# Performance work log

Measured on AMD Instinct MI355X. Metric: run time of the kernel, lower is better.

The kernel has to match this reference:

```python
import jax, jax.numpy as jnp
import numpy as np

B, MQ, MK = 8, 512, 2048
Q_DIM, KV_DIM = 1024, 256
H = 8
QKC, VC = 1024, 1024
DQ, DV = QKC // H, VC // H
EPS = 1e-5  # nn.LayerNorm default


def _layer_norm(x, w, b):
    m = jnp.mean(x, axis=-1, keepdims=True)
    v = jnp.var(x, axis=-1, keepdims=True)
    return (x - m) * jax.lax.rsqrt(v + EPS) * w + b


def setup_inputs() -> dict:
    key = jax.random.key(0)
    ks = jax.random.split(key, 12)
    hidden_states = jax.random.normal(ks[0], (B, MQ, Q_DIM), dtype=jnp.float32)
    inputs = jax.random.normal(ks[1], (B, MK, KV_DIM), dtype=jnp.float32)
    # ragged per-batch kv lengths -> prefix-valid mask (matches keys[i, :n] packing)
    lengths = jax.random.randint(ks[2], (B,), MK // 4, MK + 1)
    inputs_mask = (jnp.arange(MK)[None, :] < lengths[:, None]).astype(jnp.int32)
    s = 0.02
    return {
        "hidden_states": hidden_states,
        "inputs": inputs,
        "inputs_mask": inputs_mask,
        "ln1_w": jnp.ones((Q_DIM,), jnp.float32),
        "ln1_b": jnp.zeros((Q_DIM,), jnp.float32),
        "ln2_w": jnp.ones((KV_DIM,), jnp.float32),
        "ln2_b": jnp.zeros((KV_DIM,), jnp.float32),
        "Wq": s * jax.random.normal(ks[3], (Q_DIM, QKC), dtype=jnp.float32),
        "bq": jnp.zeros((QKC,), jnp.float32),
        "Wk": s * jax.random.normal(ks[4], (KV_DIM, QKC), dtype=jnp.float32),
        "bk": jnp.zeros((QKC,), jnp.float32),
        "Wv": s * jax.random.normal(ks[5], (KV_DIM, VC), dtype=jnp.float32),
        "bv": jnp.zeros((VC,), jnp.float32),
    }


def reference(hidden_states, inputs, inputs_mask, ln1_w, ln1_b, ln2_w, ln2_b,
              Wq, bq, Wk, bk, Wv, bv):
    hs = _layer_norm(hidden_states, ln1_w, ln1_b)      # [B, MQ, Q_DIM]
    kv = _layer_norm(inputs, ln2_w, ln2_b)             # [B, MK, KV_DIM]

    q = (hs @ Wq + bq).reshape(B, MQ, H, DQ)           # [B, MQ, H, DQ]
    k = (kv @ Wk + bk).reshape(B, MK, H, DQ)           # [B, MK, H, DQ]
    v = (kv @ Wv + bv).reshape(B, MK, H, DV)           # [B, MK, H, DV]

    scores = jnp.einsum("bqhd,bkhd->bhqk", q, k) / jnp.sqrt(jnp.float32(DQ))
    mask_f = inputs_mask.astype(scores.dtype)          # [B, MK]
    neg = jnp.finfo(scores.dtype).min
    scores = scores + (1.0 - mask_f)[:, None, None, :] * neg
    probs = jax.nn.softmax(scores, axis=-1)            # [B, H, MQ, MK]

    ctx = jnp.einsum("bhqk,bkhd->bqhd", probs, v)      # [B, MQ, H, DV]
    return ctx.reshape(B, MQ, H * DV)
```

## Files before the change

kernel.cpp:

```cpp
#include <hip/hip_runtime.h>

#define DI __device__ __forceinline__

typedef _Float16 f16x8 __attribute__((ext_vector_type(8)));
typedef _Float16 f16x4 __attribute__((ext_vector_type(4)));
typedef float    f32x4 __attribute__((ext_vector_type(4)));

namespace {

constexpr int kB  = 8;
constexpr int kMQ = 512;
constexpr int kMK = 2048;
constexpr int kQKC = 1024;
constexpr int kVC  = 1024;

DI void gload16(const void* g, void* l) {
  __builtin_amdgcn_global_load_lds(
      (const __attribute__((address_space(1))) void*)g,
      (__attribute__((address_space(3))) void*)l, 16, 0, 0);
}

DI f32x4 mfma16(f16x8 a, f16x8 b, f32x4 c) {
  return __builtin_amdgcn_mfma_f32_16x16x32_f16(a, b, c, 0, 0, 0);
}

DI f32x4 mfma16k16(f16x4 a, f16x4 b, f32x4 c) {
  return __builtin_amdgcn_mfma_f32_16x16x16f16(a, b, c, 0, 0, 0);
}

template<int K, int N>
DI void transpose_dev(const float* __restrict__ W, _Float16* __restrict__ WT,
                      int bid, float (*t)[65]) {
  int nt = bid % (N / 64), kt = bid / (N / 64);
  int k0 = kt * 64, n0 = nt * 64;
  int tid = threadIdx.x;
#pragma unroll
  for (int j = 0; j < 16; ++j) {
    int e = tid + j * 256;
    int r = e >> 6, c = e & 63;
    t[r][c] = W[(size_t)(k0 + r) * N + n0 + c];
  }
  __syncthreads();
#pragma unroll
  for (int j = 0; j < 16; ++j) {
    int e = tid + j * 256;
    int r = e >> 6, c = e & 63;
    WT[(size_t)(n0 + r) * K + k0 + c] = (_Float16)t[c][r];
  }
}

DI void ln1024_dev(const float* __restrict__ x, const float* __restrict__ w,
                   const float* __restrict__ bb, _Float16* __restrict__ y,
                   int row, float* red) {
  int tid = threadIdx.x;
  const float4* xr = (const float4*)(x + (size_t)row * 1024);
  float4 v = xr[tid];
  float s = v.x + v.y + v.z + v.w;
  float q = v.x * v.x + v.y * v.y + v.z * v.z + v.w * v.w;
#pragma unroll
  for (int m = 32; m; m >>= 1) { s += __shfl_xor(s, m); q += __shfl_xor(q, m); }
  if ((tid & 63) == 0) { red[tid >> 6] = s; red[4 + (tid >> 6)] = q; }
  __syncthreads();
  s = red[0] + red[1] + red[2] + red[3];
  q = red[4] + red[5] + red[6] + red[7];
  float mean = s * (1.0f / 1024.0f);
  float var = q * (1.0f / 1024.0f) - mean * mean;
  float inv = rsqrtf(var + 1e-5f);
  f16x4 o;
  const float* wp = w + tid * 4;
  const float* bp = bb + tid * 4;
  o[0] = (_Float16)((v.x - mean) * inv * wp[0] + bp[0]);
  o[1] = (_Float16)((v.y - mean) * inv * wp[1] + bp[1]);
  o[2] = (_Float16)((v.z - mean) * inv * wp[2] + bp[2]);
  o[3] = (_Float16)((v.w - mean) * inv * wp[3] + bp[3]);
  *(f16x4*)(y + (size_t)row * 1024 + tid * 4) = o;
}

DI void ln256_dev(const float* __restrict__ x, const float* __restrict__ w,
                  const float* __restrict__ bb, _Float16* __restrict__ y, int bid) {
  int tid = threadIdx.x;
  int lane = tid & 63, wv = tid >> 6;
  size_t row = (size_t)bid * 4 + wv;
  const float4* xr = (const float4*)(x + row * 256);
  float4 v = xr[lane];
  float s = v.x + v.y + v.z + v.w;
  float q = v.x * v.x + v.y * v.y + v.z * v.z + v.w * v.w;
#pragma unroll
  for (int m = 32; m; m >>= 1) { s += __shfl_xor(s, m); q += __shfl_xor(q, m); }
  float mean = s * (1.0f / 256.0f);
  float var = q * (1.0f / 256.0f) - mean * mean;
  float inv = rsqrtf(var + 1e-5f);
  f16x4 o;
  const float* wp = w + lane * 4;
  const float* bp = bb + lane * 4;
  o[0] = (_Float16)((v.x - mean) * inv * wp[0] + bp[0]);
  o[1] = (_Float16)((v.y - mean) * inv * wp[1] + bp[1]);
  o[2] = (_Float16)((v.z - mean) * inv * wp[2] + bp[2]);
  o[3] = (_Float16)((v.w - mean) * inv * wp[3] + bp[3]);
  *(f16x4*)(y + row * 256 + lane * 4) = o;
}

__global__ __launch_bounds__(256) void prep_all(
    const float* __restrict__ Wq, const float* __restrict__ Wk, const float* __restrict__ Wv,
    _Float16* __restrict__ WqT, _Float16* __restrict__ WkT, _Float16* __restrict__ WvT,
    const float* __restrict__ hs, const float* __restrict__ ln1w, const float* __restrict__ ln1b,
    _Float16* __restrict__ hsln,
    const float* __restrict__ xin, const float* __restrict__ ln2w, const float* __restrict__ ln2b,
    _Float16* __restrict__ kvln,
    const int* __restrict__ msk, int* __restrict__ work) {
  __shared__ float tbuf[64][65];
  int bid = blockIdx.x;
  if (bid < 256) {
    transpose_dev<1024, 1024>(Wq, WqT, bid, tbuf);
  } else if (bid < 320) {
    transpose_dev<256, 1024>(Wk, WkT, bid - 256, tbuf);
  } else if (bid < 384) {
    transpose_dev<256, 1024>(Wv, WvT, bid - 320, tbuf);
  } else if (bid < 4480) {
    ln1024_dev(hs, ln1w, ln1b, hsln, bid - 384, (float*)tbuf);
  } else if (bid < 8576) {
    ln256_dev(xin, ln2w, ln2b, kvln, bid - 4480);
  } else {
    int* wbuf = (int*)tbuf;
    int t = threadIdx.x;
    int b = t >> 5, tile = t & 31;
    wbuf[t] = (msk[b * kMK + tile * 64] != 0) ? 1 : 0;
    __syncthreads();
    if (t < 8) {
      int s = 0;
      for (int i = 0; i < 32; ++i) s += wbuf[t * 32 + i];
      wbuf[256 + t] = s;
    }
    __syncthreads();
    if (t == 0) {
      int ord[8];
      for (int i = 0; i < 8; ++i) ord[i] = i;
      for (int i = 1; i < 8; ++i) {
        int o = ord[i], j = i;
        while (j > 0 && wbuf[256 + ord[j - 1]] < wbuf[256 + o]) { ord[j] = ord[j - 1]; --j; }
        ord[j] = o;
      }
      for (int i = 0; i < 8; ++i) wbuf[264 + i] = ord[i];
    }
    __syncthreads();
#pragma unroll
    for (int k = 0; k < 4; ++k) {
      int p = t + k * 256;
      int s = p >> 7, h = p & 7, qh = (p >> 3) & 15;
      int qt = qh >> 1, half = qh & 1;
      int bb = wbuf[264 + s];
      work[p] = (bb * 8 + h) | (qt << 6) | (half << 9);
    }
  }
}

template<int M, int N, int K, bool BIAS_ROW, int MMODE>
DI void gemm_dev(const _Float16* __restrict__ A, const _Float16* __restrict__ Bt,
                 const float* __restrict__ bias, const int* __restrict__ msk,
                 _Float16* __restrict__ C, int bid,
                 _Float16 (*As)[128 * 64], _Float16 (*Bs)[128 * 64]) {
  int tid = threadIdx.x, lane = tid & 63;
  int w = tid >> 6, wr = w >> 1, wc = w & 1;
  constexpr int NT = N / 128;
  constexpr int KT = K / 64;
  int mt = bid / NT, nt = bid % NT;
  if constexpr (MMODE == 1) { if (msk[mt * 128] == 0) return; }
  if constexpr (MMODE == 2) { if (msk[nt * 128] == 0) return; }
  const int l15 = lane & 15, l4 = lane >> 4;

  f32x4 acc[4][4] = {};

  const int rS = tid >> 3;
  const int cpS = tid & 7;

  auto stage = [&](int kt, int bufi) {
#pragma unroll
    for (int j = 0; j < 4; ++j) {
      int rr = rS + j * 32;
      int cg = cpS ^ (rr & 7);
      gload16(A  + ((size_t)(mt * 128 + rr) * K + kt * 64 + cg * 8),
              (char*)As[bufi] + j * 4096 + tid * 16);
      gload16(Bt + ((size_t)(nt * 128 + rr) * K + kt * 64 + cg * 8),
              (char*)Bs[bufi] + j * 4096 + tid * 16);
    }
  };

  stage(0, 0);
  __syncthreads();

  for (int kt = 0; kt < KT; ++kt) {
    int cur = kt & 1;
    if (kt + 1 < KT) stage(kt + 1, cur ^ 1);
#pragma unroll
    for (int ss = 0; ss < 2; ++ss) {
      f16x8 a[4], b[4];
#pragma unroll
      for (int m = 0; m < 4; ++m) {
        int ra = wr * 64 + m * 16 + l15;
        int cl = ss * 4 + l4;
        a[m] = *(const f16x8*)((const char*)As[cur] + ra * 128 + ((cl ^ (ra & 7)) << 4));
        int rb = wc * 64 + m * 16 + l15;
        b[m] = *(const f16x8*)((const char*)Bs[cur] + rb * 128 + ((cl ^ (rb & 7)) << 4));
      }
#pragma unroll
      for (int m = 0; m < 4; ++m)
#pragma unroll
        for (int n = 0; n < 4; ++n)
          acc[m][n] = mfma16(a[m], b[n], acc[m][n]);
    }
    __syncthreads();
  }

#pragma unroll
  for (int m = 0; m < 4; ++m) {
#pragma unroll
    for (int n = 0; n < 4; ++n) {
      int gi0 = mt * 128 + wr * 64 + m * 16 + l4 * 4;
      int gj  = nt * 128 + wc * 64 + n * 16 + l15;
#pragma unroll
      for (int r = 0; r < 4; ++r) {
        int gi = gi0 + r;
        float v = acc[m][n][r] + (BIAS_ROW ? bias[gi] : bias[gj]);
        C[(size_t)gi * N + gj] = (_Float16)v;
      }
    }
  }
}

__global__ __launch_bounds__(256) void gemm_all(
    const _Float16* __restrict__ hsln, const _Float16* __restrict__ WqT,
    const float* __restrict__ bq, _Float16* __restrict__ qbf,
    const _Float16* __restrict__ kvln, const _Float16* __restrict__ WkT,
    const float* __restrict__ bk, _Float16* __restrict__ kbf,
    const _Float16* __restrict__ WvT, const float* __restrict__ bv,
    _Float16* __restrict__ vT, const int* __restrict__ msk) {
  __shared__ _Float16 As[2][128 * 64];
  __shared__ _Float16 Bs[2][128 * 64];
  int bid = blockIdx.x;
  if (bid < 256) {
    gemm_dev<4096, 1024, 1024, false, 0>(hsln, WqT, bq, nullptr, qbf, bid, As, Bs);
  } else if (bid < 1280) {
    gemm_dev<16384, 1024, 256, false, 1>(kvln, WkT, bk, msk, kbf, bid - 256, As, Bs);
  } else {
    gemm_dev<1024, 16384, 256, true, 2>(WvT, kvln, bv, msk, vT, bid - 1280, As, Bs);
  }
}

__global__ __launch_bounds__(256, 2) void attn_kernel(const _Float16* __restrict__ qm,
                                                      const _Float16* __restrict__ km,
                                                      const _Float16* __restrict__ vT,
                                                      const int* __restrict__ msk,
                                                      const int* __restrict__ work,
                                                      _Float16* __restrict__ pO,
                                                      float* __restrict__ pML) {
  __shared__ _Float16 Ks[2][64 * 128];
  __shared__ _Float16 Vst[2][128 * 64];

  int tid = threadIdx.x, lane = tid & 63, w = tid >> 6;
  int v = work[blockIdx.x];
  int bh = v & 63, qt = (v >> 6) & 7, half = (v >> 9) & 1;
  int h = bh & 7, b = bh >> 3;
  const int l15 = lane & 15, l4 = lane >> 4;

  int vld = (lane < 32) ? msk[b * kMK + lane * 64] : 0;
  int ntiles = __popcll(__ballot(vld != 0));
  int lv = msk[b * kMK + (ntiles - 1) * 64 + lane];
  int lastlen = __popcll(__ballot(lv != 0));

  int h1 = (ntiles + 1) >> 1;
  int t0 = half ? h1 : 0;
  int t1 = half ? ntiles : h1;

  f16x8 qf[4];
#pragma unroll
  for (int kc = 0; kc < 4; ++kc)
    qf[kc] = *(const f16x8*)(qm +
        (size_t)(b * kMQ + qt * 64 + w * 16 + l15) * kQKC +
        h * 128 + kc * 32 + l4 * 8);

  f32x4 o[8] = {};
  float rm = -1e30f, rl = 0.0f;

  const float sl2 = 0.08838834764831845f * 1.4426950408889634f;

  const int rK = tid >> 4, cpK = tid & 15;
  const int rV = tid >> 3, cpV = tid & 7;

  auto stage = [&](int kt, int bufi) {
#pragma unroll
    for (int j = 0; j < 4; ++j) {
      int rr = rK + j * 16;
      int cg = cpK ^ (rr & 7);
      gload16(km + (size_t)(b * kMK + kt * 64 + rr) * kQKC + h * 128 + cg * 8,
              (char*)Ks[bufi] + j * 4096 + tid * 16);
    }
#pragma unroll
    for (int j = 0; j < 4; ++j) {
      int dv = rV + j * 32;
      int cg = cpV ^ (dv & 7);
      gload16(vT + (size_t)(h * 128 + dv) * (kB * kMK) + (size_t)b * kMK + kt * 64 + cg * 8,
              (char*)Vst[bufi] + j * 4096 + tid * 16);
    }
  };

  stage(t0, 0);
  __syncthreads();

  for (int kt = t0; kt < t1; ++kt) {
    int cur = (kt - t0) & 1;
    if (kt + 1 < t1) stage(kt + 1, cur ^ 1);

    f32x4 sc[4] = {};
    __builtin_amdgcn_s_setprio(1);
#pragma unroll
    for (int kc = 0; kc < 4; ++kc) {
      f16x8 kb[4];
#pragma unroll
      for (int kf = 0; kf < 4; ++kf) {
        int rr = kf * 16 + l15;
        int cl = kc * 4 + l4;
        kb[kf] = *(const f16x8*)((const char*)Ks[cur] + rr * 256 + ((cl ^ (rr & 7)) << 4));
      }
#pragma unroll
      for (int kf = 0; kf < 4; ++kf)
        sc[kf] = mfma16(kb[kf], qf[kc], sc[kf]);
    }
    __builtin_amdgcn_s_setprio(0);

    if (kt == ntiles - 1) {
#pragma unroll
      for (int kf = 0; kf < 4; ++kf)
#pragma unroll
        for (int r = 0; r < 4; ++r)
          if (kf * 16 + l4 * 4 + r >= lastlen) sc[kf][r] = -3e38f;
    }

    float mx = sc[0][0];
#pragma unroll
    for (int kf = 0; kf < 4; ++kf)
#pragma unroll
      for (int r = 0; r < 4; ++r) mx = fmaxf(mx, sc[kf][r]);
    mx = fmaxf(mx, __shfl_xor(mx, 16));
    mx = fmaxf(mx, __shfl_xor(mx, 32));
    float al = 1.0f;
    if (__any(mx > rm)) {
      float nm = fmaxf(rm, mx);
      al = __builtin_amdgcn_exp2f((rm - nm) * sl2);
      rm = nm;
#pragma unroll
      for (int n = 0; n < 8; ++n)
#pragma unroll
        for (int r = 0; r < 4; ++r) o[n][r] *= al;
    }
    float nms = rm * sl2;
    float ts = 0.0f;
#pragma unroll
    for (int kf = 0; kf < 4; ++kf)
#pragma unroll
      for (int r = 0; r < 4; ++r) {
        float p = __builtin_amdgcn_exp2f(sc[kf][r] * sl2 - nms);
        sc[kf][r] = p;
        ts += p;
      }
    ts += __shfl_xor(ts, 16);
    ts += __shfl_xor(ts, 32);
    rl = rl * al + ts;

    f16x4 pb[4];
#pragma unroll
    for (int kf = 0; kf < 4; ++kf)
#pragma unroll
      for (int r = 0; r < 4; ++r) pb[kf][r] = (_Float16)sc[kf][r];

    __builtin_amdgcn_s_setprio(1);
#pragma unroll
    for (int n = 0; n < 8; ++n) {
      int dv = n * 16 + l15;
#pragma unroll
      for (int kf = 0; kf < 4; ++kf) {
        int phys = (kf * 2 + (l4 >> 1)) ^ (l15 & 7);
        f16x4 vb = *(const f16x4*)((const char*)Vst[cur] +
                                   dv * 128 + (phys << 4) + (l4 & 1) * 8);
        o[n] = mfma16k16(vb, pb[kf], o[n]);
      }
    }
    __builtin_amdgcn_s_setprio(0);
    __syncthreads();
  }

  int item = bh * 16 + qt * 2 + half;
  _Float16* po = pO + (size_t)item * 8192;
  int qr = w * 16 + l15;
#pragma unroll
  for (int n = 0; n < 8; ++n) {
    f16x4 st;
#pragma unroll
    for (int r = 0; r < 4; ++r) st[r] = (_Float16)o[n][r];
    *(f16x4*)(po + qr * 128 + n * 16 + l4 * 4) = st;
  }
  if (l4 == 0) {
    pML[(item * 64 + qr) * 2 + 0] = rm;
    pML[(item * 64 + qr) * 2 + 1] = rl;
  }
}

__global__ __launch_bounds__(256) void combine_kernel(const _Float16* __restrict__ pO,
                                                      const float* __restrict__ pML,
                                                      float* __restrict__ out) {
  int cid = blockIdx.x;
  int bh = cid & 63, qt = cid >> 6;
  int h = bh & 7, b = bh >> 3;
  int t = threadIdx.x;
  int q = t >> 2, c = t & 3;
  const float sl2 = 0.08838834764831845f * 1.4426950408889634f;

  int i1 = bh * 16 + qt * 2, i2 = i1 + 1;
  float m1 = pML[(i1 * 64 + q) * 2 + 0], l1 = pML[(i1 * 64 + q) * 2 + 1];
  float m2 = pML[(i2 * 64 + q) * 2 + 0], l2 = pML[(i2 * 64 + q) * 2 + 1];
  float m = fmaxf(m1, m2);
  float w1 = __builtin_amdgcn_exp2f((m1 - m) * sl2);
  float w2 = __builtin_amdgcn_exp2f((m2 - m) * sl2);
  float inv = 1.0f / (l1 * w1 + l2 * w2);
  w1 *= inv; w2 *= inv;

  const _Float16* p1 = pO + (size_t)i1 * 8192 + q * 128;
  const _Float16* p2 = pO + (size_t)i2 * 8192 + q * 128;
  float* orow = out + ((size_t)b * kMQ + qt * 64 + q) * kVC + h * 128;
#pragma unroll
  for (int j = 0; j < 4; ++j) {
    int col = c * 32 + j * 8;
    f16x8 a = *(const f16x8*)(p1 + col);
    f16x8 bb = *(const f16x8*)(p2 + col);
    f32x4 o0, o1;
#pragma unroll
    for (int r = 0; r < 4; ++r) {
      o0[r] = (float)a[r] * w1 + (float)bb[r] * w2;
      o1[r] = (float)a[4 + r] * w1 + (float)bb[4 + r] * w2;
    }
    *(f32x4*)(orow + col) = o0;
    *(f32x4*)(orow + col + 4) = o1;
  }
}

}

extern "C" void kernel_launch(void* const* d_in, const int* in_sizes, int n_in,
                              void* d_out, int out_size, void* d_ws, size_t ws_size,
                              hipStream_t stream) {
  (void)in_sizes; (void)n_in; (void)out_size; (void)ws_size;
  const float* hs   = (const float*)d_in[0];
  const float* xin  = (const float*)d_in[1];
  const int*   msk  = (const int*)d_in[2];
  const float* ln1w = (const float*)d_in[3];
  const float* ln1b = (const float*)d_in[4];
  const float* ln2w = (const float*)d_in[5];
  const float* ln2b = (const float*)d_in[6];
  const float* Wq   = (const float*)d_in[7];
  const float* bq   = (const float*)d_in[8];
  const float* Wk   = (const float*)d_in[9];
  const float* bk   = (const float*)d_in[10];
  const float* Wv   = (const float*)d_in[11];
  const float* bv   = (const float*)d_in[12];
  float* out = (float*)d_out;

  char* ws = (char*)d_ws;
  _Float16* qbf  = (_Float16*)(ws + 0);
  _Float16* kbf  = (_Float16*)(ws + 8388608);
  _Float16* vT   = (_Float16*)(ws + 41943040);
  _Float16* hsln = (_Float16*)(ws + 75497472);
  _Float16* kvln = (_Float16*)(ws + 83886080);
  _Float16* WqT  = (_Float16*)(ws + 92274688);
  _Float16* WkT  = (_Float16*)(ws + 94371840);
  _Float16* WvT  = (_Float16*)(ws + 94896128);
  int*      work = (int*)(ws + 95420416);
  _Float16* pO   = hsln;
  float*    pML  = (float*)WqT;

  prep_all<<<8577, 256, 0, stream>>>(Wq, Wk, Wv, WqT, WkT, WvT,
                                     hs, ln1w, ln1b, hsln,
                                     xin, ln2w, ln2b, kvln,
                                     msk, work);
  gemm_all<<<2304, 256, 0, stream>>>(hsln, WqT, bq, qbf,
                                     kvln, WkT, bk, kbf,
                                     WvT, bv, vT, msk);
  attn_kernel<<<1024, 256, 0, stream>>>(qbf, kbf, vT, msk, work, pO, pML);
  combine_kernel<<<512, 256, 0, stream>>>(pO, pML, out);
}
```

Measured before the change: 123.0 us.

## Fuse split-K combine into attention via atomic counter; read V directly from global

The separate combine kernel is removed. Whichever of the two split halves finishes last, detected through an atomic counter that prep_all zeroes, merges both partial outputs inside the attention kernel. V tiles are no longer staged through LDS; each lane reads its f16x4 V fragments straight from global memory (vT). This halves LDS use, which allows launch bounds of 4 blocks per SM. It saves one kernel launch and the LDS copy, at the cost of uncoalesced, strided global V reads that depend on cache hits, plus fence and atomic overhead.

```diff
diff --git a/kernel.cpp b/kernel.cpp
--- a/kernel.cpp
+++ b/kernel.cpp
@@ -107,7 +107,7 @@
     _Float16* __restrict__ hsln,
     const float* __restrict__ xin, const float* __restrict__ ln2w, const float* __restrict__ ln2b,
     _Float16* __restrict__ kvln,
-    const int* __restrict__ msk, int* __restrict__ work) {
+    const int* __restrict__ msk, int* __restrict__ work, int* __restrict__ cnt) {
   __shared__ float tbuf[64][65];
   int bid = blockIdx.x;
   if (bid < 256) {
@@ -123,6 +123,8 @@
   } else {
     int* wbuf = (int*)tbuf;
     int t = threadIdx.x;
+    cnt[t] = 0;
+    cnt[256 + t] = 0;
     int b = t >> 5, tile = t & 31;
     wbuf[t] = (msk[b * kMK + tile * 64] != 0) ? 1 : 0;
     __syncthreads();
@@ -246,15 +248,17 @@
   }
 }
 
-__global__ __launch_bounds__(256, 2) void attn_kernel(const _Float16* __restrict__ qm,
+__global__ __launch_bounds__(256, 4) void attn_kernel(const _Float16* __restrict__ qm,
                                                       const _Float16* __restrict__ km,
                                                       const _Float16* __restrict__ vT,
                                                       const int* __restrict__ msk,
                                                       const int* __restrict__ work,
                                                       _Float16* __restrict__ pO,
-                                                      float* __restrict__ pML) {
+                                                      float* __restrict__ pML,
+                                                      int* __restrict__ cnt,
+                                                      float* __restrict__ out) {
   __shared__ _Float16 Ks[2][64 * 128];
-  __shared__ _Float16 Vst[2][128 * 64];
+  __shared__ int flag;
 
   int tid = threadIdx.x, lane = tid & 63, w = tid >> 6;
   int v = work[blockIdx.x];
@@ -284,7 +288,6 @@
   const float sl2 = 0.08838834764831845f * 1.4426950408889634f;
 
   const int rK = tid >> 4, cpK = tid & 15;
-  const int rV = tid >> 3, cpV = tid & 7;
 
   auto stage = [&](int kt, int bufi) {
 #pragma unroll
@@ -294,14 +297,9 @@
       gload16(km + (size_t)(b * kMK + kt * 64 + rr) * kQKC + h * 128 + cg * 8,
               (char*)Ks[bufi] + j * 4096 + tid * 16);
     }
-#pragma unroll
-    for (int j = 0; j < 4; ++j) {
-      int dv = rV + j * 32;
-      int cg = cpV ^ (dv & 7);
-      gload16(vT + (size_t)(h * 128 + dv) * (kB * kMK) + (size_t)b * kMK + kt * 64 + cg * 8,
-              (char*)Vst[bufi] + j * 4096 + tid * 16);
-    }
   };
+
+  const _Float16* vbase = vT + (size_t)h * 128 * (kB * kMK) + (size_t)b * kMK;
 
   stage(t0, 0);
   __syncthreads();
@@ -375,12 +373,10 @@
     __builtin_amdgcn_s_setprio(1);
 #pragma unroll
     for (int n = 0; n < 8; ++n) {
-      int dv = n * 16 + l15;
+      const _Float16* vrow = vbase + (size_t)(n * 16 + l15) * (kB * kMK) + kt * 64 + l4 * 4;
 #pragma unroll
       for (int kf = 0; kf < 4; ++kf) {
-        int phys = (kf * 2 + (l4 >> 1)) ^ (l15 & 7);
-        f16x4 vb = *(const f16x4*)((const char*)Vst[cur] +
-                                   dv * 128 + (phys << 4) + (l4 & 1) * 8);
+        f16x4 vb = *(const f16x4*)(vrow + kf * 16);
         o[n] = mfma16k16(vb, pb[kf], o[n]);
       }
     }
@@ -402,19 +398,15 @@
     pML[(item * 64 + qr) * 2 + 0] = rm;
     pML[(item * 64 + qr) * 2 + 1] = rl;
   }
-}
-
-__global__ __launch_bounds__(256) void combine_kernel(const _Float16* __restrict__ pO,
-                                                      const float* __restrict__ pML,
-                                                      float* __restrict__ out) {
-  int cid = blockIdx.x;
-  int bh = cid & 63, qt = cid >> 6;
-  int h = bh & 7, b = bh >> 3;
-  int t = threadIdx.x;
-  int q = t >> 2, c = t & 3;
-  const float sl2 = 0.08838834764831845f * 1.4426950408889634f;
+
+  __threadfence();
+  if (tid == 0) flag = atomicAdd(&cnt[bh * 8 + qt], 1);
+  __syncthreads();
+  if (flag != 1) return;
+  __threadfence();
 
   int i1 = bh * 16 + qt * 2, i2 = i1 + 1;
+  int q = tid >> 2, c = tid & 3;
   float m1 = pML[(i1 * 64 + q) * 2 + 0], l1 = pML[(i1 * 64 + q) * 2 + 1];
   float m2 = pML[(i2 * 64 + q) * 2 + 0], l2 = pML[(i2 * 64 + q) * 2 + 1];
   float m = fmaxf(m1, m2);
@@ -430,12 +422,12 @@
   for (int j = 0; j < 4; ++j) {
     int col = c * 32 + j * 8;
     f16x8 a = *(const f16x8*)(p1 + col);
-    f16x8 bb = *(const f16x8*)(p2 + col);
+    f16x8 bb2 = *(const f16x8*)(p2 + col);
     f32x4 o0, o1;
 #pragma unroll
     for (int r = 0; r < 4; ++r) {
-      o0[r] = (float)a[r] * w1 + (float)bb[r] * w2;
-      o1[r] = (float)a[4 + r] * w1 + (float)bb[4 + r] * w2;
+      o0[r] = (float)a[r] * w1 + (float)bb2[r] * w2;
+      o1[r] = (float)a[4 + r] * w1 + (float)bb2[4 + r] * w2;
     }
     *(f32x4*)(orow + col) = o0;
     *(f32x4*)(orow + col + 4) = o1;
@@ -473,16 +465,16 @@
   _Float16* WkT  = (_Float16*)(ws + 94371840);
   _Float16* WvT  = (_Float16*)(ws + 94896128);
   int*      work = (int*)(ws + 95420416);
+  int*      cnt  = (int*)(ws + 95424512);
   _Float16* pO   = hsln;
   float*    pML  = (float*)WqT;
 
   prep_all<<<8577, 256, 0, stream>>>(Wq, Wk, Wv, WqT, WkT, WvT,
                                      hs, ln1w, ln1b, hsln,
                                      xin, ln2w, ln2b, kvln,
-                                     msk, work);
+                                     msk, work, cnt);
   gemm_all<<<2304, 256, 0, stream>>>(hsln, WqT, bq, qbf,
                                      kvln, WkT, bk, kbf,
                                      WvT, bv, vT, msk);
-  attn_kernel<<<1024, 256, 0, stream>>>(qbf, kbf, vT, msk, work, pO, pML);
-  combine_kernel<<<512, 256, 0, stream>>>(pO, pML, out);
-}
+  attn_kernel<<<1024, 256, 0, stream>>>(qbf, kbf, vT, msk, work, pO, pML, cnt, out);
+}
```

Result: slower. 392.4 us (+218.9%).
